# Kernel tuning notes

Measured on AMD Instinct MI355X. Metric: run time of the kernel, lower is better.

## Reference

```python
import jax, jax.numpy as jnp
import numpy as np

EMBED = 256
HEADS = 8
N, L, S = 4, 128, 64


def setup_inputs() -> dict:
    key = jax.random.key(0)
    ks = jax.random.split(key, 9)
    values = jax.random.normal(ks[0], (N, L, S, EMBED), dtype=jnp.float32)
    keys_ = jax.random.normal(ks[1], (N, L, S, EMBED), dtype=jnp.float32)
    query = jax.random.normal(ks[2], (N, L, S, EMBED), dtype=jnp.float32)
    mask = jax.random.randint(ks[3], (N, 1, L, L, 1), 0, 2, dtype=jnp.int32)
    sc = 1.0 / np.sqrt(EMBED)
    Wq = jax.random.normal(ks[4], (EMBED, EMBED), dtype=jnp.float32) * sc
    Wk = jax.random.normal(ks[5], (EMBED, EMBED), dtype=jnp.float32) * sc
    Wv = jax.random.normal(ks[6], (EMBED, EMBED), dtype=jnp.float32) * sc
    Wo = jax.random.normal(ks[7], (HEADS * EMBED, EMBED), dtype=jnp.float32) * (1.0 / np.sqrt(HEADS * EMBED))
    bo = jnp.zeros((EMBED,), dtype=jnp.float32)
    return {"values": values, "keys": keys_, "query": query, "mask": mask,
            "Wq": Wq, "Wk": Wk, "Wv": Wv, "Wo": Wo, "bo": bo}


def reference(values, keys, query, mask, Wq, Wk, Wv, Wo, bo):
    n, q_len, s_len, d = query.shape
    k_len = keys.shape[1]
    h = HEADS
    # Per-head projections share one weight (expand happens BEFORE Linear in
    # the original), so compute each projection once and broadcast over heads.
    q = jnp.einsum('nqsd,de->nqse', query, Wq)   # [N,Q,S,D]
    k = jnp.einsum('nksd,de->nkse', keys, Wk)    # [N,K,S,D]
    v = jnp.einsum('nksd,de->nkse', values, Wv)  # [N,K,S,D]
    # energy: nqshd,nkshd->nhqks ; identical across h pre-mask
    energy = jnp.einsum('nqsd,nksd->nqks', q, k)            # [N,Q,K,S]
    energy = jnp.broadcast_to(energy[:, None], (n, h, q_len, k_len, s_len))
    energy = jnp.where(mask == 0, jnp.float32(-1e20), energy)
    attn = jax.nn.softmax(energy / jnp.sqrt(jnp.float32(d)), axis=3)  # over K
    # out: nhqls,nlshd->nqshd
    out = jnp.einsum('nhqks,nksd->nqshd', attn, v)
    out = out.reshape(n, q_len, s_len, h * d)
    return out @ Wo + bo
```

## Files before the change

### kernel.cpp

```cpp
#include <hip/hip_runtime.h>
#include <hip/hip_bf16.h>


using bf16x4 = __attribute__((ext_vector_type(4))) __bf16;
using bf16x8 = __attribute__((ext_vector_type(8))) __bf16;
using f32x16 = __attribute__((ext_vector_type(16))) float;

#define MFMA32(a, b, c) __builtin_amdgcn_mfma_f32_32x32x16_bf16((a), (b), (c), 0, 0, 0)

__device__ __forceinline__ bf16x8 cvt8(float4 f0, float4 f1) {
  bf16x8 a;
  a[0]=(__bf16)f0.x; a[1]=(__bf16)f0.y; a[2]=(__bf16)f0.z; a[3]=(__bf16)f0.w;
  a[4]=(__bf16)f1.x; a[5]=(__bf16)f1.y; a[6]=(__bf16)f1.z; a[7]=(__bf16)f1.w;
  return a;
}
__device__ __forceinline__ f32x16 zero16() {
  f32x16 z;
#pragma unroll
  for (int j = 0; j < 16; ++j) z[j] = 0.f;
  return z;
}
__device__ __forceinline__ unsigned pk(float a, float b) {
  union { __bf16 h[2]; unsigned u; } x;
  x.h[0] = (__bf16)a; x.h[1] = (__bf16)b;
  return x.u;
}
__device__ __forceinline__ bf16x8 u4frag(uint4 w) {
  union { uint4 u; bf16x8 f; } x;
  x.u = w;
  return x.f;
}
__device__ __forceinline__ uint4 mkfrag(const float* a8, int hl) {
  unsigned p00 = pk(a8[0], a8[1]), p01 = pk(a8[2], a8[3]);
  unsigned p10 = pk(a8[4], a8[5]), p11 = pk(a8[6], a8[7]);
  unsigned r0 = __shfl_xor((int)(hl ? p00 : p10), 32);
  unsigned r1 = __shfl_xor((int)(hl ? p01 : p11), 32);
  uint4 w;
  w.x = hl ? r0 : p00;  w.y = hl ? r1 : p01;
  w.z = hl ? p10 : r0;  w.w = hl ? p11 : r1;
  return w;
}

__global__ __launch_bounds__(512) void prep_pack(
    const float* __restrict__ Wq, const float* __restrict__ Wk,
    const float* __restrict__ Wv, const float* __restrict__ Wo,
    const int* __restrict__ mask,
    __bf16* __restrict__ mqk, __bf16* __restrict__ mvo,
    unsigned* __restrict__ mbits) {
  __shared__ float wt[256 * 33];
  const int t = threadIdx.x, lane = t & 63, w = t >> 6;
  const int lq = lane & 31, hl = lane >> 5;
  const int ct = blockIdx.x;
  const bool isV = blockIdx.y != 0;
  if (!isV) {
    int gid = ct * 512 + t;
    if (gid < 2048) {
      const int* mrow = mask + gid * 32;
      unsigned mw = 0;
#pragma unroll
      for (int b = 0; b < 32; ++b) mw |= (mrow[b] != 0 ? 1u : 0u) << b;
      mbits[gid] = mw;
    }
  } else {
#pragma unroll
    for (int i = 0; i < 16; ++i) {
      int cell = i * 512 + t;
      int e2 = cell >> 5, eol = cell & 31;
      float ssum = 0.f;
#pragma unroll
      for (int h = 0; h < 8; ++h)
        ssum += Wo[((size_t)(h * 256 + e2)) * 256 + ct * 32 + eol];
      wt[e2 * 33 + eol] = ssum;
    }
    __syncthreads();
  }
  const float* Aw = isV ? Wv : Wq;
  bf16x8 afr[16], bfr[16];
#pragma unroll
  for (int ks = 0; ks < 16; ++ks) {
    const float* p = Aw + (size_t)(w * 32 + lq) * 256 + ks * 16 + hl * 8;
    afr[ks] = cvt8(*(const float4*)p, *(const float4*)(p + 4));
  }
  if (!isV) {
#pragma unroll
    for (int ks = 0; ks < 16; ++ks) {
      const float* p = Wk + (size_t)(ct * 32 + lq) * 256 + ks * 16 + hl * 8;
      bfr[ks] = cvt8(*(const float4*)p, *(const float4*)(p + 4));
    }
  } else {
#pragma unroll
    for (int ks = 0; ks < 16; ++ks)
#pragma unroll
      for (int jj = 0; jj < 8; ++jj)
        bfr[ks][jj] = (__bf16)wt[(ks * 16 + hl * 8 + jj) * 33 + lq];
  }
  f32x16 acc = zero16();
#pragma unroll
  for (int ks = 0; ks < 16; ++ks) acc = MFMA32(afr[ks], bfr[ks], acc);
  char* dstb = (char*)(isV ? mvo : mqk);
#pragma unroll
  for (int a = 0; a < 4; ++a) {
    bf16x4 v;
#pragma unroll
    for (int j = 0; j < 4; ++j) v[j] = (__bf16)acc[4 * a + j];
    *(bf16x4*)(dstb + ct * 16384 + (2 * w + (a >> 1)) * 1024 +
               (lq + 32 * (a & 1)) * 16 + hl * 8) = v;
  }
}

__global__ __launch_bounds__(512) void fused_attn(
    const float* __restrict__ Xv, const float* __restrict__ Xk,
    const float* __restrict__ Xq, const unsigned* __restrict__ mbits,
    const __bf16* __restrict__ mqk, const __bf16* __restrict__ mvo,
    const float* __restrict__ bo, float* __restrict__ out) {
  extern __shared__ char lds[];
  char* A     = lds;
  char* Timg  = lds + 65536;
  char* Pimg  = lds + 65536;
  float* scr  = (float*)(lds + 98304);
  const int t = threadIdx.x, lane = t & 63, w = t >> 6;
  const int lq = lane & 31, hl = lane >> 5;
  const int qt = w & 3, kh = w >> 2;
  const int sl = blockIdx.x, n = sl >> 6, s = sl & 63;

  auto fill = [&](const float* __restrict__ X, float4* vr) {
#pragma unroll
    for (int i = 0; i < 8; ++i) {
      int f8 = i * 512 + t, row = f8 >> 5, c8 = f8 & 31;
      const float* src = X + ((size_t)(n * 8192 + row * 64 + s)) * 256 + c8 * 8;
      vr[2 * i]     = *reinterpret_cast<const float4*>(src);
      vr[2 * i + 1] = *reinterpret_cast<const float4*>(src + 4);
    }
  };
  auto flushv = [&](const float4* vr) {
#pragma unroll
    for (int i = 0; i < 8; ++i) {
      int f8 = i * 512 + t, row = f8 >> 5, c8 = f8 & 31;
      bf16x8 b;
      b[0]=(__bf16)vr[2*i].x;   b[1]=(__bf16)vr[2*i].y;
      b[2]=(__bf16)vr[2*i].z;   b[3]=(__bf16)vr[2*i].w;
      b[4]=(__bf16)vr[2*i+1].x; b[5]=(__bf16)vr[2*i+1].y;
      b[6]=(__bf16)vr[2*i+1].z; b[7]=(__bf16)vr[2*i+1].w;
      *reinterpret_cast<bf16x8*>(A + row * 512 + ((c8 * 16) ^ ((row & 15) << 4))) = b;
    }
  };
  auto xfrag = [&](int brow, int ks) -> bf16x8 {
    return *reinterpret_cast<const bf16x8*>(
        A + brow * 512 + ((ks * 32 + hl * 16) ^ ((brow & 15) << 4)));
  };

  bf16x8 wf[16];
  {
    const bf16x8* wp = reinterpret_cast<const bf16x8*>(mqk);
#pragma unroll
    for (int ks = 0; ks < 16; ++ks) wf[ks] = wp[(w * 16 + ks) * 64 + lane];
  }
  float4 vrp[16];
  {
    float4 vr[16];
    fill(Xq, vr);
    fill(Xk, vrp);
    flushv(vr);
  }
  __syncthreads();

#pragma unroll
  for (int rt = 0; rt < 4; ++rt) {
    f32x16 acc = zero16();
#pragma unroll
    for (int ks = 0; ks < 16; ++ks)
      acc = MFMA32(wf[ks], xfrag(rt * 32 + lq, ks), acc);
#pragma unroll
    for (int s16 = 0; s16 < 2; ++s16) {
      float a8[8];
#pragma unroll
      for (int i = 0; i < 8; ++i) a8[i] = acc[8 * s16 + i];
      uint4 wd = mkfrag(a8, hl);
      *(uint4*)(Timg + rt * 16384 + (2 * w + s16) * 1024 + lane * 16) = wd;
    }
  }
  __syncthreads();

  bf16x8 af[16];
#pragma unroll
  for (int ks = 0; ks < 16; ++ks)
    af[ks] = *reinterpret_cast<const bf16x8*>(Timg + qt * 16384 + ks * 1024 + lane * 16);
  flushv(vrp);
  fill(Xv, vrp);
  __syncthreads();

  unsigned mw0 = mbits[((size_t)n * 128 + qt * 32 + lq) * 4 + 2 * kh];
  unsigned mw1 = mbits[((size_t)n * 128 + qt * 32 + lq) * 4 + 2 * kh + 1];
  f32x16 acc[2];
#pragma unroll
  for (int c = 0; c < 2; ++c) {
    acc[c] = zero16();
    int kt = 2 * kh + c;
#pragma unroll
    for (int ks = 0; ks < 16; ++ks)
      acc[c] = MFMA32(xfrag(kt * 32 + lq, ks), af[ks], acc[c]);
  }
  float mx = -3e38f;
#pragma unroll
  for (int c = 0; c < 2; ++c) {
    unsigned mw = c ? mw1 : mw0;
#pragma unroll
    for (int r = 0; r < 16; ++r) {
      int bit = (r & 3) + 8 * (r >> 2) + 4 * hl;
      float sv = ((mw >> bit) & 1u) ? acc[c][r] * 0.0625f : -6.25e18f;
      acc[c][r] = sv;
      mx = fmaxf(mx, sv);
    }
  }
  mx = fmaxf(mx, __shfl_xor(mx, 32));
  float sum = 0.f;
#pragma unroll
  for (int c = 0; c < 2; ++c)
#pragma unroll
    for (int r = 0; r < 16; ++r) {
      float e = __expf(acc[c][r] - mx);
      acc[c][r] = e;
      sum += e;
    }
  sum += __shfl_xor(sum, 32);
  if (lane < 32) {
    float2* s2 = reinterpret_cast<float2*>(scr);
    s2[(qt * 2 + kh) * 32 + lane] = make_float2(mx, sum);
  }
  __syncthreads();

  {
    float2 pr = reinterpret_cast<const float2*>(scr)[(qt * 2 + (kh ^ 1)) * 32 + lq];
    float M = fmaxf(mx, pr.x);
    float tot = sum * __expf(mx - M) + pr.y * __expf(pr.x - M);
    float scale = __expf(mx - M) / tot;
#pragma unroll
    for (int c = 0; c < 2; ++c)
#pragma unroll
      for (int r = 0; r < 16; ++r) acc[c][r] *= scale;
  }
  bf16x8 vf[16];
  {
    const bf16x8* vp = reinterpret_cast<const bf16x8*>(mvo);
#pragma unroll
    for (int ks = 0; ks < 16; ++ks) vf[ks] = vp[(w * 16 + ks) * 64 + lane];
  }
#pragma unroll
  for (int c = 0; c < 2; ++c) {
    int kt = 2 * kh + c;
#pragma unroll
    for (int s16 = 0; s16 < 2; ++s16) {
      float a8[8];
#pragma unroll
      for (int i = 0; i < 8; ++i) a8[i] = acc[c][8 * s16 + i];
      uint4 wd = mkfrag(a8, hl);
      *(uint4*)(Pimg + qt * 8192 + (kt * 2 + s16) * 1024 + lane * 16) = wd;
    }
  }
  flushv(vrp);
  __syncthreads();

  bf16x8 afB1[8];
#pragma unroll
  for (int rt = 0; rt < 4; ++rt) {
    f32x16 a1 = zero16();
#pragma unroll
    for (int ks = 0; ks < 16; ++ks)
      a1 = MFMA32(xfrag(rt * 32 + lq, ks), vf[ks], a1);
#pragma unroll
    for (int s16 = 0; s16 < 2; ++s16) {
      float a8[8];
#pragma unroll
      for (int i = 0; i < 8; ++i) a8[i] = a1[8 * s16 + i];
      afB1[rt * 2 + s16] = u4frag(mkfrag(a8, hl));
    }
  }

#pragma unroll
  for (int q4 = 0; q4 < 4; ++q4) {
    f32x16 a2 = zero16();
#pragma unroll
    for (int ks = 0; ks < 8; ++ks) {
      bf16x8 pfr = *reinterpret_cast<const bf16x8*>(
          Pimg + q4 * 8192 + ks * 1024 + lane * 16);
      a2 = MFMA32(afB1[ks], pfr, a2);
    }
    float* orow = out + ((size_t)(n * 8192) + (q4 * 32 + lq) * 64 + s) * 256;
#pragma unroll
    for (int a = 0; a < 4; ++a) {
      float4 bv = *reinterpret_cast<const float4*>(bo + w * 32 + 8 * a + 4 * hl);
      float4 st;
      st.x = a2[4*a]   + bv.x; st.y = a2[4*a+1] + bv.y;
      st.z = a2[4*a+2] + bv.z; st.w = a2[4*a+3] + bv.w;
      *reinterpret_cast<float4*>(orow + w * 32 + 8 * a + 4 * hl) = st;
    }
  }
}

extern "C" void kernel_launch(void* const* d_in, const int* in_sizes, int n_in,
                              void* d_out, int out_size, void* d_ws, size_t ws_size,
                              hipStream_t stream) {
  const float* values = (const float*)d_in[0];
  const float* keys   = (const float*)d_in[1];
  const float* query  = (const float*)d_in[2];
  const int*   mask   = (const int*)d_in[3];
  const float* Wq     = (const float*)d_in[4];
  const float* Wk     = (const float*)d_in[5];
  const float* Wv     = (const float*)d_in[6];
  const float* Wo     = (const float*)d_in[7];
  const float* bo     = (const float*)d_in[8];
  float* out = (float*)d_out;

  char* w = (char*)d_ws;
  __bf16*   mqk   = (__bf16*)w;   w += 131072;
  __bf16*   mvo   = (__bf16*)w;   w += 131072;
  unsigned* mbits = (unsigned*)w; w += 8192;

  prep_pack<<<dim3(8, 2), 512, 0, stream>>>(Wq, Wk, Wv, Wo, mask, mqk, mvo, mbits);
  fused_attn<<<256, 512, 131072, stream>>>(values, keys, query, mbits,
                                           mqk, mvo, bo, out);
}
```

Measured before the change: 56.35 us.

## Split each slice across two blocks by query half to double grid size

Each (n,s) slice now runs as two 256-thread blocks, each handling 64 of the 128 query rows, giving 512 blocks instead of 256, with less LDS per block (80KB) so two blocks can share a CU. Each block still has to project the full K and V (128 rows), so the K and V projection work is duplicated across the pair. K and V are streamed in two 64-row halves, which adds syncs. The aim is better CU coverage and occupancy on a GPU with more CUs than the old grid had blocks, at the cost of redundant K/V loads and projection math.

```diff
diff --git a/kernel.cpp b/kernel.cpp
--- a/kernel.cpp
+++ b/kernel.cpp
@@ -108,34 +108,36 @@
   }
 }
 
-__global__ __launch_bounds__(512) void fused_attn(
+__global__ __launch_bounds__(256, 2) void fused_attn(
     const float* __restrict__ Xv, const float* __restrict__ Xk,
     const float* __restrict__ Xq, const unsigned* __restrict__ mbits,
     const __bf16* __restrict__ mqk, const __bf16* __restrict__ mvo,
     const float* __restrict__ bo, float* __restrict__ out) {
   extern __shared__ char lds[];
-  char* A     = lds;
-  char* Timg  = lds + 65536;
-  char* Pimg  = lds + 65536;
-  float* scr  = (float*)(lds + 98304);
+  char* A    = lds;
+  char* Timg = lds + 32768;
+  char* Pimg = lds + 65536;
   const int t = threadIdx.x, lane = t & 63, w = t >> 6;
   const int lq = lane & 31, hl = lane >> 5;
-  const int qt = w & 3, kh = w >> 2;
-  const int sl = blockIdx.x, n = sl >> 6, s = sl & 63;
-
-  auto fill = [&](const float* __restrict__ X, float4* vr) {
+  const int qt = w & 1, kh = w >> 1;
+  const int bx = blockIdx.x;
+  const int sl = bx & 255, qh = bx >> 8;
+  const int n = sl >> 6, s = sl & 63;
+
+  auto fillh = [&](const float* __restrict__ X, int grow0, float4* vr) {
 #pragma unroll
     for (int i = 0; i < 8; ++i) {
-      int f8 = i * 512 + t, row = f8 >> 5, c8 = f8 & 31;
-      const float* src = X + ((size_t)(n * 8192 + row * 64 + s)) * 256 + c8 * 8;
+      int f8 = i * 256 + t, row = f8 >> 5, c8 = f8 & 31;
+      const float* src =
+          X + ((size_t)(n * 8192 + (grow0 + row) * 64 + s)) * 256 + c8 * 8;
       vr[2 * i]     = *reinterpret_cast<const float4*>(src);
       vr[2 * i + 1] = *reinterpret_cast<const float4*>(src + 4);
     }
   };
-  auto flushv = [&](const float4* vr) {
+  auto flushh = [&](const float4* vr, int lrow0) {
 #pragma unroll
     for (int i = 0; i < 8; ++i) {
-      int f8 = i * 512 + t, row = f8 >> 5, c8 = f8 & 31;
+      int f8 = i * 256 + t, row = lrow0 + (f8 >> 5), c8 = f8 & 31;
       bf16x8 b;
       b[0]=(__bf16)vr[2*i].x;   b[1]=(__bf16)vr[2*i].y;
       b[2]=(__bf16)vr[2*i].z;   b[3]=(__bf16)vr[2*i].w;
@@ -149,48 +151,54 @@
         A + brow * 512 + ((ks * 32 + hl * 16) ^ ((brow & 15) << 4)));
   };
 
-  bf16x8 wf[16];
+  bf16x8 wf[2][16];
   {
     const bf16x8* wp = reinterpret_cast<const bf16x8*>(mqk);
 #pragma unroll
-    for (int ks = 0; ks < 16; ++ks) wf[ks] = wp[(w * 16 + ks) * 64 + lane];
-  }
-  float4 vrp[16];
-  {
-    float4 vr[16];
-    fill(Xq, vr);
-    fill(Xk, vrp);
-    flushv(vr);
-  }
-  __syncthreads();
-
-#pragma unroll
-  for (int rt = 0; rt < 4; ++rt) {
-    f32x16 acc = zero16();
-#pragma unroll
-    for (int ks = 0; ks < 16; ++ks)
-      acc = MFMA32(wf[ks], xfrag(rt * 32 + lq, ks), acc);
-#pragma unroll
-    for (int s16 = 0; s16 < 2; ++s16) {
-      float a8[8];
-#pragma unroll
-      for (int i = 0; i < 8; ++i) a8[i] = acc[8 * s16 + i];
-      uint4 wd = mkfrag(a8, hl);
-      *(uint4*)(Timg + rt * 16384 + (2 * w + s16) * 1024 + lane * 16) = wd;
-    }
-  }
+    for (int dtl = 0; dtl < 2; ++dtl)
+#pragma unroll
+      for (int ks = 0; ks < 16; ++ks)
+        wf[dtl][ks] = wp[((2 * w + dtl) * 16 + ks) * 64 + lane];
+  }
+  float4 vr[16];
+  fillh(Xq, qh * 64, vr);
+  flushh(vr, 0);
+  fillh(Xk, 0, vr);
+  __syncthreads();
+
+#pragma unroll
+  for (int rt = 0; rt < 2; ++rt)
+#pragma unroll
+    for (int dtl = 0; dtl < 2; ++dtl) {
+      f32x16 acc = zero16();
+#pragma unroll
+      for (int ks = 0; ks < 16; ++ks)
+        acc = MFMA32(wf[dtl][ks], xfrag(rt * 32 + lq, ks), acc);
+#pragma unroll
+      for (int s16 = 0; s16 < 2; ++s16) {
+        float a8[8];
+#pragma unroll
+        for (int i = 0; i < 8; ++i) a8[i] = acc[8 * s16 + i];
+        *(uint4*)(Timg + rt * 16384 + ((2 * w + dtl) * 2 + s16) * 1024 +
+                  lane * 16) = mkfrag(a8, hl);
+      }
+    }
   __syncthreads();
 
   bf16x8 af[16];
 #pragma unroll
   for (int ks = 0; ks < 16; ++ks)
     af[ks] = *reinterpret_cast<const bf16x8*>(Timg + qt * 16384 + ks * 1024 + lane * 16);
-  flushv(vrp);
-  fill(Xv, vrp);
-  __syncthreads();
-
-  unsigned mw0 = mbits[((size_t)n * 128 + qt * 32 + lq) * 4 + 2 * kh];
-  unsigned mw1 = mbits[((size_t)n * 128 + qt * 32 + lq) * 4 + 2 * kh + 1];
+  flushh(vr, 0);
+  fillh(Xk, 64, vr);
+  __syncthreads();
+  flushh(vr, 64);
+  fillh(Xv, 0, vr);
+  __syncthreads();
+
+  const int qglob = qh * 64 + qt * 32 + lq;
+  unsigned mw0 = mbits[((size_t)n * 128 + qglob) * 4 + 2 * kh];
+  unsigned mw1 = mbits[((size_t)n * 128 + qglob) * 4 + 2 * kh + 1];
   f32x16 acc[2];
 #pragma unroll
   for (int c = 0; c < 2; ++c) {
@@ -223,14 +231,16 @@
       sum += e;
     }
   sum += __shfl_xor(sum, 32);
-  if (lane < 32) {
-    float2* s2 = reinterpret_cast<float2*>(scr);
-    s2[(qt * 2 + kh) * 32 + lane] = make_float2(mx, sum);
-  }
-  __syncthreads();
-
+  if (lane < 32)
+    *reinterpret_cast<float2*>(Pimg + qt * 8192 + kh * 4096 + lane * 8) =
+        make_float2(mx, sum);
+  __syncthreads();
+
+  float4 vr2[16];
+  fillh(Xv, 64, vr2);
   {
-    float2 pr = reinterpret_cast<const float2*>(scr)[(qt * 2 + (kh ^ 1)) * 32 + lq];
+    float2 pr = *reinterpret_cast<const float2*>(
+        Pimg + qt * 8192 + (kh ^ 1) * 4096 + lq * 8);
     float M = fmaxf(mx, pr.x);
     float tot = sum * __expf(mx - M) + pr.y * __expf(pr.x - M);
     float scale = __expf(mx - M) / tot;
@@ -239,62 +249,72 @@
 #pragma unroll
       for (int r = 0; r < 16; ++r) acc[c][r] *= scale;
   }
-  bf16x8 vf[16];
+  __syncthreads();
+
+#pragma unroll
+  for (int c = 0; c < 2; ++c)
+#pragma unroll
+    for (int s16 = 0; s16 < 2; ++s16) {
+      float a8[8];
+#pragma unroll
+      for (int i = 0; i < 8; ++i) a8[i] = acc[c][8 * s16 + i];
+      *(uint4*)(Pimg + qt * 8192 + ((2 * kh + c) * 2 + s16) * 1024 + lane * 16) =
+          mkfrag(a8, hl);
+    }
+  flushh(vr, 0);
+  flushh(vr2, 64);
+  bf16x8 vf[2][16];
   {
     const bf16x8* vp = reinterpret_cast<const bf16x8*>(mvo);
 #pragma unroll
-    for (int ks = 0; ks < 16; ++ks) vf[ks] = vp[(w * 16 + ks) * 64 + lane];
-  }
-#pragma unroll
-  for (int c = 0; c < 2; ++c) {
-    int kt = 2 * kh + c;
-#pragma unroll
-    for (int s16 = 0; s16 < 2; ++s16) {
-      float a8[8];
-#pragma unroll
-      for (int i = 0; i < 8; ++i) a8[i] = acc[c][8 * s16 + i];
-      uint4 wd = mkfrag(a8, hl);
-      *(uint4*)(Pimg + qt * 8192 + (kt * 2 + s16) * 1024 + lane * 16) = wd;
-    }
-  }
-  flushv(vrp);
-  __syncthreads();
-
-  bf16x8 afB1[8];
-#pragma unroll
-  for (int rt = 0; rt < 4; ++rt) {
-    f32x16 a1 = zero16();
-#pragma unroll
-    for (int ks = 0; ks < 16; ++ks)
-      a1 = MFMA32(xfrag(rt * 32 + lq, ks), vf[ks], a1);
-#pragma unroll
-    for (int s16 = 0; s16 < 2; ++s16) {
-      float a8[8];
-#pragma unroll
-      for (int i = 0; i < 8; ++i) a8[i] = a1[8 * s16 + i];
-      afB1[rt * 2 + s16] = u4frag(mkfrag(a8, hl));
-    }
-  }
-
-#pragma unroll
-  for (int q4 = 0; q4 < 4; ++q4) {
-    f32x16 a2 = zero16();
-#pragma unroll
-    for (int ks = 0; ks < 8; ++ks) {
-      bf16x8 pfr = *reinterpret_cast<const bf16x8*>(
-          Pimg + q4 * 8192 + ks * 1024 + lane * 16);
-      a2 = MFMA32(afB1[ks], pfr, a2);
-    }
-    float* orow = out + ((size_t)(n * 8192) + (q4 * 32 + lq) * 64 + s) * 256;
-#pragma unroll
-    for (int a = 0; a < 4; ++a) {
-      float4 bv = *reinterpret_cast<const float4*>(bo + w * 32 + 8 * a + 4 * hl);
-      float4 st;
-      st.x = a2[4*a]   + bv.x; st.y = a2[4*a+1] + bv.y;
-      st.z = a2[4*a+2] + bv.z; st.w = a2[4*a+3] + bv.w;
-      *reinterpret_cast<float4*>(orow + w * 32 + 8 * a + 4 * hl) = st;
-    }
-  }
+    for (int etl = 0; etl < 2; ++etl)
+#pragma unroll
+      for (int ks = 0; ks < 16; ++ks)
+        vf[etl][ks] = vp[((2 * w + etl) * 16 + ks) * 64 + lane];
+  }
+  __syncthreads();
+
+  bf16x8 afB1[2][8];
+#pragma unroll
+  for (int etl = 0; etl < 2; ++etl)
+#pragma unroll
+    for (int rt = 0; rt < 4; ++rt) {
+      f32x16 a1 = zero16();
+#pragma unroll
+      for (int ks = 0; ks < 16; ++ks)
+        a1 = MFMA32(xfrag(rt * 32 + lq, ks), vf[etl][ks], a1);
+#pragma unroll
+      for (int s16 = 0; s16 < 2; ++s16) {
+        float a8[8];
+#pragma unroll
+        for (int i = 0; i < 8; ++i) a8[i] = a1[8 * s16 + i];
+        afB1[etl][rt * 2 + s16] = u4frag(mkfrag(a8, hl));
+      }
+    }
+
+#pragma unroll
+  for (int q4 = 0; q4 < 2; ++q4)
+#pragma unroll
+    for (int etl = 0; etl < 2; ++etl) {
+      f32x16 a2 = zero16();
+#pragma unroll
+      for (int ks = 0; ks < 8; ++ks) {
+        bf16x8 pfr = *reinterpret_cast<const bf16x8*>(
+            Pimg + q4 * 8192 + ks * 1024 + lane * 16);
+        a2 = MFMA32(afB1[etl][ks], pfr, a2);
+      }
+      int et = 2 * w + etl;
+      float* orow =
+          out + ((size_t)(n * 8192) + (qh * 64 + q4 * 32 + lq) * 64 + s) * 256;
+#pragma unroll
+      for (int a = 0; a < 4; ++a) {
+        float4 bv = *reinterpret_cast<const float4*>(bo + et * 32 + 8 * a + 4 * hl);
+        float4 st;
+        st.x = a2[4*a]   + bv.x; st.y = a2[4*a+1] + bv.y;
+        st.z = a2[4*a+2] + bv.z; st.w = a2[4*a+3] + bv.w;
+        *reinterpret_cast<float4*>(orow + et * 32 + 8 * a + 4 * hl) = st;
+      }
+    }
 }
 
 extern "C" void kernel_launch(void* const* d_in, const int* in_sizes, int n_in,
@@ -317,6 +337,6 @@
   unsigned* mbits = (unsigned*)w; w += 8192;
 
   prep_pack<<<dim3(8, 2), 512, 0, stream>>>(Wq, Wk, Wv, Wo, mask, mqk, mvo, mbits);
-  fused_attn<<<256, 512, 131072, stream>>>(values, keys, query, mbits,
-                                           mqk, mvo, bo, out);
-}
+  fused_attn<<<512, 256, 81920, stream>>>(values, keys, query, mbits,
+                                          mqk, mvo, bo, out);
+}
```

Measured after the change: 111.2 us. 97.3% more time.
